# Optimization experiments

Hardware: AMD Instinct MI355X
Metric: run time of the kernel (lower is better)

The kernel has to match this reference:

```python
import jax, jax.numpy as jnp
import numpy as np
import math

E = 256      # embed_dim
H = 16       # num_heads
D = E // H   # qkv_dim
MSH = 16     # ms_hidden_dim
B, R, C = 2, 512, 512


def setup_inputs() -> dict:
    key = jax.random.key(0)
    ks = jax.random.split(key, 10)
    x1 = jax.random.normal(ks[0], (B, R, E), jnp.float32)
    x2 = jax.random.normal(ks[1], (B, C, E), jnp.float32)
    attn_mask = jax.random.randint(ks[2], (B, R, C), 0, 2) > 0  # True = valid
    cost_mat = jax.random.uniform(ks[3], (B, R, C), jnp.float32)
    # torch nn.Linear default init ~ U(-1/sqrt(fan_in), 1/sqrt(fan_in))
    def lin(k, out_d, in_d, bound):
        return jax.random.uniform(k, (out_d, in_d), jnp.float32, -bound, bound)
    Wqv1 = lin(ks[4], 2 * E, E, 1.0 / math.sqrt(E))
    Wkv2 = lin(ks[5], 2 * E, E, 1.0 / math.sqrt(E))
    W1 = lin(ks[6], H * MSH, 2 * H, math.sqrt(0.5))       # mix1_init
    W2 = lin(ks[7], H, H * MSH, math.sqrt(1.0 / MSH))      # mix2_init
    Wout1 = lin(ks[8], E, E, 1.0 / math.sqrt(E))
    Wout2 = lin(ks[9], E, E, 1.0 / math.sqrt(E))
    return {"x1": x1, "x2": x2, "attn_mask": attn_mask, "cost_mat": cost_mat,
            "Wqv1": Wqv1, "Wkv2": Wkv2, "W1": W1, "W2": W2,
            "Wout1": Wout1, "Wout2": Wout2}


def _apply_weights_and_combine(logits, v, mask):
    # mask: True = masked out; rows fully masked are un-masked (torch clone trick)
    all_masked = jnp.all(mask, axis=-1, keepdims=True)
    mask = jnp.where(all_masked, False, mask)
    logits = jnp.where(mask, -jnp.inf, logits)
    w = jax.nn.softmax(logits, axis=-1)          # [b,h,r,c]
    out = jnp.einsum('bhrc,bhcd->bhrd', w, v)     # [b,h,r,d]
    b, h, r, d = out.shape
    return out.transpose(0, 2, 1, 3).reshape(b, r, h * d)  # b s (h d)


def reference(x1, x2, attn_mask, cost_mat, Wqv1, Wkv2, W1, W2, Wout1, Wout2):
    b, r, _ = x1.shape
    c = x2.shape[1]
    # q, v1 from x1 ; k, v2 from x2
    qv = (x1 @ Wqv1.T).reshape(b, r, 2, H, D)
    q = qv[:, :, 0].transpose(0, 2, 1, 3)   # [b,h,r,d]
    v1 = qv[:, :, 1].transpose(0, 2, 1, 3)
    kv = (x2 @ Wkv2.T).reshape(b, c, 2, H, D)
    k = kv[:, :, 0].transpose(0, 2, 1, 3)   # [b,h,c,d]
    v2 = kv[:, :, 1].transpose(0, 2, 1, 3)

    dot = jnp.einsum('bhrd,bhcd->bhrc', q, k) * (1.0 / math.sqrt(D))
    cost = jnp.broadcast_to(cost_mat[:, None], dot.shape)  # [b,h,r,c]

    # MixedScoreFF: stack -> [b,h,r,c,2] -> [b,r,c,2h] -> MLP -> [b,r,c,h]
    two = jnp.stack((dot, cost), axis=-1)
    two = two.transpose(0, 2, 3, 1, 4).reshape(b, r, c, 2 * H)
    ms = jax.nn.relu(two @ W1.T) @ W2.T      # [b,r,c,H]
    ms1 = ms.transpose(0, 3, 1, 2)            # [b,h,r,c]
    ms2 = ms1.transpose(0, 1, 3, 2)           # [b,h,c,r]

    mask1 = jnp.broadcast_to(~attn_mask[:, None], (b, H, r, c))  # True = masked
    mask2 = mask1.transpose(0, 1, 3, 2)

    h1 = _apply_weights_and_combine(ms1, v2, mask1) @ Wout1.T  # [b,r,E]
    h2 = _apply_weights_and_combine(ms2, v1, mask2) @ Wout2.T  # [b,c,E]
    return (h1, h2)
```

## Files before the change

### kernel.cpp

```cpp
#include <hip/hip_runtime.h>
#include <hip/hip_bf16.h>

typedef unsigned int   u32;
typedef unsigned short u16;

typedef __attribute__((ext_vector_type(8))) short    sh8;
typedef __attribute__((ext_vector_type(4))) float    f32x4;
typedef __attribute__((ext_vector_type(8))) _Float16 f16x8;
typedef __attribute__((ext_vector_type(2))) _Float16 f16x2;
typedef __attribute__((ext_vector_type(2))) __fp16   fp16x2raw;

union F16x8 { f16x8 v; uint4 u; f16x2 p[4]; _Float16 h[8]; };
union F16x4u { uint2 u; _Float16 h[4]; };
union F16x2u { u32 u; _Float16 h[2]; };
union CvtU  { fp16x2raw r; f16x2 p; u32 u; };

__device__ __forceinline__ float b2f(u16 u) { union { u32 i; float f; } v; v.i = ((u32)u) << 16; return v.f; }
__device__ __forceinline__ u16   f2b(float f){
  union { float f; u32 i; } v; v.f = f;
  u32 u = v.i;
  u32 r = (u + 0x7fffu + ((u >> 16) & 1u)) >> 16;
  return (u16)r;
}
__device__ __forceinline__ u32 pk2(float a, float b) {
  __hip_bfloat162 h2 = __float22bfloat162_rn(make_float2(a, b));
  union { __hip_bfloat162 h; u32 u; } v; v.h = h2; return v.u;
}
__device__ __forceinline__ f16x2 cvtpk(float a, float b) {
  CvtU c; c.r = __builtin_amdgcn_cvt_pkrtz(a, b); return c.p;
}
__device__ __forceinline__ u32 cvtpku(float a, float b) {
  CvtU c; c.r = __builtin_amdgcn_cvt_pkrtz(a, b); return c.u;
}

__device__ __forceinline__ f32x4 mfma16(uint4 a, uint4 b, f32x4 c) {
  union { uint4 u; sh8 s; } ua, ub;
  ua.u = a; ub.u = b;
  return __builtin_amdgcn_mfma_f32_16x16x32_bf16(ua.s, ub.s, c, 0, 0, 0);
}
__device__ __forceinline__ f32x4 mfma32h(f16x8 a, f16x8 b, f32x4 c) {
  return __builtin_amdgcn_mfma_f32_16x16x32_f16(a, b, c, 0, 0, 0);
}

__device__ __forceinline__ void split8(float4 v0, float4 v1, uint4& hi, uint4& lo) {
  float a[8] = {v0.x, v0.y, v0.z, v0.w, v1.x, v1.y, v1.z, v1.w};
  u32 hw[4], lw[4];
#pragma unroll
  for (int t = 0; t < 4; t++) {
    u32 hp = pk2(a[2 * t], a[2 * t + 1]);
    float r0 = a[2 * t]     - __uint_as_float(hp << 16);
    float r1 = a[2 * t + 1] - __uint_as_float(hp & 0xffff0000u);
    hw[t] = hp;
    lw[t] = pk2(r0, r1);
  }
  hi = make_uint4(hw[0], hw[1], hw[2], hw[3]);
  lo = make_uint4(lw[0], lw[1], lw[2], lw[3]);
}

__global__ void __launch_bounds__(256)
gemm_mf(const float* __restrict__ A0, const float* __restrict__ B0, float* __restrict__ C0,
        const float* __restrict__ A1, const float* __restrict__ B1, float* __restrict__ C1,
        int N, int K) {
  int t = threadIdx.x, L = t & 63, w = t >> 6;
  int cl = L & 15, q = L >> 4;
  int by = blockIdx.y, sel = by >> 4;
  const float* A  = sel ? A1 : A0;
  const float* Bw = sel ? B1 : B0;
  float*       C  = sel ? C1 : C0;
  int m0 = (by & 15) * 64 + w * 16;
  int n0 = blockIdx.x * 16;

  f32x4 acc; acc[0] = 0.f; acc[1] = 0.f; acc[2] = 0.f; acc[3] = 0.f;
  const float* ar = A  + (size_t)(m0 + cl) * K + 8 * q;
  const float* br = Bw + (size_t)(n0 + cl) * K + 8 * q;

  for (int k0 = 0; k0 < K; k0 += 32) {
    float4 av0 = *(const float4*)(ar + k0);
    float4 av1 = *(const float4*)(ar + k0 + 4);
    float4 bv0 = *(const float4*)(br + k0);
    float4 bv1 = *(const float4*)(br + k0 + 4);
    uint4 ahi, alo, bhi, blo;
    split8(av0, av1, ahi, alo);
    split8(bv0, bv1, bhi, blo);
    acc = mfma16(ahi, bhi, acc);
    acc = mfma16(ahi, blo, acc);
    acc = mfma16(alo, bhi, acc);
  }
#pragma unroll
  for (int i = 0; i < 4; i++)
    C[(size_t)(m0 + 4 * q + i) * N + n0 + cl] = acc[i];
}

__global__ void __launch_bounds__(256)
gemm_mf_pack(const float* __restrict__ x1, const float* __restrict__ Wqv1, u16* __restrict__ vh1,
             const float* __restrict__ x2, const float* __restrict__ Wkv2, u16* __restrict__ vh2,
             const float* __restrict__ W1, const float* __restrict__ W2,
             uint4* __restrict__ QQ4, uint4* __restrict__ KH4, uint4* __restrict__ KL4z,
             uint4* __restrict__ W1F8hi, uint4* __restrict__ W1F8lo,
             uint4* __restrict__ W2F8hi, uint4* __restrict__ W2F8lo) {
  __shared__ float Ld[4][16][17];
  int t = threadIdx.x, L = t & 63, w = t >> 6;
  int cl = L & 15, q = L >> 4;
  int by = blockIdx.y;

  if (by == 32) {
    if (blockIdx.x >= 8) return;
    int tid = blockIdx.x * 256 + t;
    if (tid < 1024) {
      int LL = tid & 63, nt = tid >> 6;
      int j = nt * 16 + (LL & 15), qq = LL >> 4;
      F16x8 hi, lo;
#pragma unroll
      for (int jj = 0; jj < 8; jj++) {
        float wv = W1[j * 32 + qq * 8 + jj];
        hi.h[jj] = (_Float16)wv;
        lo.h[jj] = (_Float16)(wv - (float)hi.h[jj]);
      }
      W1F8hi[tid] = hi.u;
      W1F8lo[tid] = lo.u;
    } else if (tid < 1536) {
      int t2 = tid - 1024;
      int LL = t2 & 63, p = t2 >> 6;
      int h = LL & 15, qq = LL >> 4;
      F16x8 hi, lo;
#pragma unroll
      for (int jj = 0; jj < 8; jj++) {
        int j = 32 * p + ((jj >> 2) << 4) + 4 * qq + (jj & 3);
        float wv = W2[h * 256 + j];
        hi.h[jj] = (_Float16)wv;
        lo.h[jj] = (_Float16)(wv - (float)hi.h[jj]);
      }
      W2F8hi[t2] = hi.u;
      W2F8lo[t2] = lo.u;
    }
    return;
  }

  int sel = by >> 4;
  const float* A  = sel ? x2 : x1;
  const float* Bw = sel ? Wkv2 : Wqv1;
  int m0 = (by & 15) * 64 + w * 16;
  int n0 = blockIdx.x * 16;

  f32x4 acc; acc[0] = 0.f; acc[1] = 0.f; acc[2] = 0.f; acc[3] = 0.f;
  const float* ar = A  + (size_t)(m0 + cl) * 256 + 8 * q;
  const float* br = Bw + (size_t)(n0 + cl) * 256 + 8 * q;

  for (int k0 = 0; k0 < 256; k0 += 32) {
    float4 av0 = *(const float4*)(ar + k0);
    float4 av1 = *(const float4*)(ar + k0 + 4);
    float4 bv0 = *(const float4*)(br + k0);
    float4 bv1 = *(const float4*)(br + k0 + 4);
    uint4 ahi, alo, bhi, blo;
    split8(av0, av1, ahi, alo);
    split8(bv0, bv1, bhi, blo);
    acc = mfma16(ahi, bhi, acc);
    acc = mfma16(ahi, blo, acc);
    acc = mfma16(alo, bhi, acc);
  }

  int b = m0 >> 9;
  int row = (m0 & 511) + cl;

  if (n0 >= 256) {
#pragma unroll
    for (int i = 0; i < 4; i++) Ld[w][cl][4 * q + i] = acc[i];
    if (q < 2) {
      float v[8];
#pragma unroll
      for (int jj = 0; jj < 8; jj++) v[jj] = Ld[w][q * 8 + jj][cl];
      uint4 o = make_uint4(cvtpku(v[0], v[1]), cvtpku(v[2], v[3]),
                           cvtpku(v[4], v[5]), cvtpku(v[6], v[7]));
      u16* vh = sel ? vh2 : vh1;
      *(uint4*)(vh + ((size_t)(b * 512) + row) * 256 + (n0 - 256) + q * 8) = o;
    }
    return;
  }

#pragma unroll
  for (int i = 0; i < 4; i++) Ld[w][cl][4 * q + i] = acc[i];
  float v[8];
#pragma unroll
  for (int jj = 0; jj < 8; jj++) v[jj] = Ld[w][(q & 1) * 8 + jj][cl];

  int r = row;
  int h = n0 >> 4;

  if (sel == 0) {
    u32 wv[4];
#pragma unroll
    for (int t2 = 0; t2 < 4; t2++) {
      float a  = v[2 * t2] * 0.25f, bb = v[2 * t2 + 1] * 0.25f;
      u32 hp = pk2(a, bb);
      if (q >= 2) {
        float r0 = a  - __uint_as_float(hp << 16);
        float r1 = bb - __uint_as_float(hp & 0xffff0000u);
        wv[t2] = pk2(r0, r1);
      } else wv[t2] = hp;
    }
    QQ4[((size_t)((b * 16 + h) * 4 + q) << 9) + r] = make_uint4(wv[0], wv[1], wv[2], wv[3]);
  } else {
    u32 hw[4], lw[4];
#pragma unroll
    for (int t2 = 0; t2 < 4; t2++) {
      float a = v[2 * t2], bb = v[2 * t2 + 1];
      u32 hp = pk2(a, bb);
      float r0 = a  - __uint_as_float(hp << 16);
      float r1 = bb - __uint_as_float(hp & 0xffff0000u);
      hw[t2] = hp;
      lw[t2] = pk2(r0, r1);
    }
    if (q < 2) {
      KH4[((size_t)((b * 16 + h) * 2 + q) << 9) + r]       = make_uint4(hw[0], hw[1], hw[2], hw[3]);
      KL4z[((size_t)((b * 16 + h) * 4 + 2 + q) << 9) + r]  = make_uint4(0, 0, 0, 0);
    } else {
      KL4z[((size_t)((b * 16 + h) * 4 + (q - 2)) << 9) + r] = make_uint4(lw[0], lw[1], lw[2], lw[3]);
    }
  }
}

__global__ void __launch_bounds__(256, 4)
ms_mfma8c(const uint4* __restrict__ QQ4, const uint4* __restrict__ KH4,
          const uint4* __restrict__ KL4z, const float* __restrict__ cost,
          const uint4* __restrict__ W1F8hi, const uint4* __restrict__ W1F8lo,
          const uint4* __restrict__ W2F8hi, const uint4* __restrict__ W2F8lo,
          u16* __restrict__ ms1, u16* __restrict__ ms2) {
  __shared__ __align__(16) u32 Dl[2 * 2176];
  int t = threadIdx.x, L = t & 63, w = t >> 6;
  int cl = L & 15, q = L >> 4;
  int b = blockIdx.z, c0 = blockIdx.x * 16;
  int pairId = w >> 1, wl = w & 1;
  int r0a = blockIdx.y * 32 + pairId * 16;
  int r0  = r0a + wl * 8;
  u32* D = Dl + pairId * 2176;

  f32x4 z; z[0] = 0.f; z[1] = 0.f; z[2] = 0.f; z[3] = 0.f;

#pragma unroll 2
  for (int hpi = 0; hpi < 4; hpi++) {
    int hp = wl * 4 + hpi;
    int h0 = 2 * hp, h1 = 2 * hp + 1;
    uint4 qa  = QQ4[((size_t)((b * 16 + h0) * 4 + q) << 9) + r0a + cl];
    uint4 qa2 = QQ4[((size_t)((b * 16 + h0) * 4 + (q & 1)) << 9) + r0a + cl];
    uint4 kb1 = KH4[((size_t)((b * 16 + h0) * 2 + (q & 1)) << 9) + c0 + cl];
    uint4 kb2 = KL4z[((size_t)((b * 16 + h0) * 4 + q) << 9) + c0 + cl];
    f32x4 d0 = mfma16(qa, kb1, z);
    d0 = mfma16(qa2, kb2, d0);
    uint4 qb  = QQ4[((size_t)((b * 16 + h1) * 4 + q) << 9) + r0a + cl];
    uint4 qb2 = QQ4[((size_t)((b * 16 + h1) * 4 + (q & 1)) << 9) + r0a + cl];
    uint4 kc1 = KH4[((size_t)((b * 16 + h1) * 2 + (q & 1)) << 9) + c0 + cl];
    uint4 kc2 = KL4z[((size_t)((b * 16 + h1) * 4 + q) << 9) + c0 + cl];
    f32x4 d1 = mfma16(qb, kc1, z);
    d1 = mfma16(qb2, kc2, d1);
#pragma unroll
    for (int i = 0; i < 4; i++)
      D[(4 * q + i) * 136 + hp * 17 + cl] = cvtpku(d0[i], d1[i]);
  }
  __syncthreads();

  F16x8 xv[8];
#pragma unroll
  for (int rr = 0; rr < 8; rr++) {
    int rl = wl * 8 + rr;
    float cv = cost[((size_t)(b * 512) + r0 + rr) * 512 + c0 + cl];
    u32 ch = cvtpku(0.f, cv);
    u32 ua = D[rl * 136 + (2 * q) * 17 + cl];
    u32 ub = D[rl * 136 + (2 * q + 1) * 17 + cl];
    xv[rr].u = make_uint4((ua & 0xffffu) | ch, (ua >> 16) | ch,
                          (ub & 0xffffu) | ch, (ub >> 16) | ch);
  }

  f32x4 acc2[8];
#pragma unroll
  for (int rr = 0; rr < 8; rr++) acc2[rr] = z;

#pragma unroll 1
  for (int p = 0; p < 8; p++) {
    F16x8 w1h0, w1h1, w2h, w2l;
    w1h0.u = W1F8hi[(2 * p) * 64 + L];
    w1h1.u = W1F8hi[(2 * p + 1) * 64 + L];
    w2h.u  = W2F8hi[p * 64 + L];
    w2l.u  = W2F8lo[p * 64 + L];
#pragma unroll
    for (int rr = 0; rr < 8; rr++) {
      f32x4 a0 = mfma32h(w1h0.v, xv[rr].v, z);
      f32x4 a1 = mfma32h(w1h1.v, xv[rr].v, z);
      F16x8 hf;
      hf.p[0] = cvtpk(fmaxf(a0[0], 0.f), fmaxf(a0[1], 0.f));
      hf.p[1] = cvtpk(fmaxf(a0[2], 0.f), fmaxf(a0[3], 0.f));
      hf.p[2] = cvtpk(fmaxf(a1[0], 0.f), fmaxf(a1[1], 0.f));
      hf.p[3] = cvtpk(fmaxf(a1[2], 0.f), fmaxf(a1[3], 0.f));
      acc2[rr] = mfma32h(hf.v, w2h.v, acc2[rr]);
      acc2[rr] = mfma32h(hf.v, w2l.v, acc2[rr]);
    }
  }

  u32* ms1u = (u32*)ms1;
#pragma unroll
  for (int rr = 0; rr < 8; rr++) {
    size_t base = ((size_t)(b * 16 + cl) * 512 + (r0 + rr)) * 256 + (c0 >> 1) + q * 2;
    ms1u[base]     = pk2(acc2[rr][0], acc2[rr][1]);
    ms1u[base + 1] = pk2(acc2[rr][2], acc2[rr][3]);
  }
  u32* ms2u = (u32*)ms2;
#pragma unroll
  for (int i = 0; i < 4; i++) {
    int c = c0 + 4 * q + i;
    u32 o[4];
#pragma unroll
    for (int j = 0; j < 4; j++)
      o[j] = pk2(acc2[2 * j][i], acc2[2 * j + 1][i]);
    size_t base2 = ((size_t)(b * 16 + cl) * 512 + c) * 256 + (r0 >> 1);
    *(uint4*)&ms2u[base2] = make_uint4(o[0], o[1], o[2], o[3]);
  }
}

__global__ void __launch_bounds__(256)
softmax_all5b(const u16* __restrict__ ms1s, const u16* __restrict__ ms2s,
              const int* __restrict__ mask,
              const u16* __restrict__ vh1, const u16* __restrict__ vh2,
              float* __restrict__ o1, float* __restrict__ o2) {
  __shared__ _Float16 pbuf[512 * 16 * 2];
  __shared__ float    sden[2][16];
  __shared__ float4   red[4][64];
  int t = threadIdx.x, lane = t & 63, w = t >> 6;
  int fix0 = blockIdx.x * 2, b = blockIdx.y, dir = blockIdx.z;
  const u16* ms   = dir ? ms2s : ms1s;
  const u16* vbuf = dir ? vh1 : vh2;
  float*     obuf = dir ? o2 : o1;

  int fsel = w >> 1;
  int fix  = fix0 + fsel;
  int hbase = (w & 1) * 8;
  bool vd[8];
#pragma unroll
  for (int i = 0; i < 8; i++) {
    int cc = i * 64 + lane;
    int mv = dir ? mask[((size_t)b * 512 + cc) * 512 + fix]
                 : mask[((size_t)b * 512 + fix) * 512 + cc];
    vd[i] = mv != 0;
  }
  bool anyl = false;
#pragma unroll
  for (int i = 0; i < 8; i++) anyl |= vd[i];
  bool useMask = (__ballot(anyl) != 0ULL);

#pragma unroll 2
  for (int h2 = 0; h2 < 8; h2++) {
    int h = hbase + h2;
    const u16* mrow = ms + ((size_t)(b * 16 + h) * 512 + fix) * 512;
    float lg[8];
#pragma unroll
    for (int i = 0; i < 8; i++) lg[i] = b2f(mrow[i * 64 + lane]);
    float mx = -3.4e38f;
#pragma unroll
    for (int i = 0; i < 8; i++)
      if (!(useMask && !vd[i])) mx = fmaxf(mx, lg[i]);
    for (int off = 32; off; off >>= 1) mx = fmaxf(mx, __shfl_xor(mx, off));
    float s = 0.f;
#pragma unroll
    for (int i = 0; i < 8; i++) {
      float p = (useMask && !vd[i]) ? 0.f : __expf(lg[i] - mx);
      int cc = i * 64 + lane;
      pbuf[(cc * 16 + ((h + cc) & 15)) * 2 + fsel] = (_Float16)p;
      s += p;
    }
    for (int off = 32; off; off >>= 1) s += __shfl_xor(s, off);
    if (lane == 0) sden[fsel][h] = s;
  }
  __syncthreads();

  int hb = lane >> 2, dq = lane & 3;
  const u16* vb = vbuf + (size_t)b * 131072 + hb * 16 + dq * 4;
  float4 acc0 = make_float4(0.f, 0.f, 0.f, 0.f);
  float4 acc1 = make_float4(0.f, 0.f, 0.f, 0.f);
  for (int it = 0; it < 128; it++) {
    int cc = it * 4 + w;
    F16x4u vv; vv.u = *(const uint2*)(vb + (size_t)cc * 256);
    F16x2u pv; pv.u = *(const u32*)&pbuf[(cc * 16 + ((hb + cc) & 15)) * 2];
    float v0 = (float)vv.h[0], v1 = (float)vv.h[1];
    float v2 = (float)vv.h[2], v3 = (float)vv.h[3];
    float p0 = (float)pv.h[0], p1 = (float)pv.h[1];
    acc0.x += p0 * v0; acc0.y += p0 * v1; acc0.z += p0 * v2; acc0.w += p0 * v3;
    acc1.x += p1 * v0; acc1.y += p1 * v1; acc1.z += p1 * v2; acc1.w += p1 * v3;
  }
#pragma unroll 1
  for (int f = 0; f < 2; f++) {
    red[w][lane] = f ? acc1 : acc0;
    __syncthreads();
    if (w == 0) {
      float4 s0 = red[0][lane], s1 = red[1][lane];
      float4 s2 = red[2][lane], s3 = red[3][lane];
      float inv = 1.f / sden[f][hb];
      float4 o;
      o.x = (s0.x + s1.x + s2.x + s3.x) * inv;
      o.y = (s0.y + s1.y + s2.y + s3.y) * inv;
      o.z = (s0.z + s1.z + s2.z + s3.z) * inv;
      o.w = (s0.w + s1.w + s2.w + s3.w) * inv;
      *(float4*)(obuf + ((size_t)b * 512 + fix0 + f) * 256 + lane * 4) = o;
    }
    __syncthreads();
  }
}

extern "C" void kernel_launch(void* const* d_in, const int* in_sizes, int n_in,
                              void* d_out, int out_size, void* d_ws, size_t ws_size,
                              hipStream_t stream) {
  const float* x1    = (const float*)d_in[0];
  const float* x2    = (const float*)d_in[1];
  const int*   attn  = (const int*)d_in[2];
  const float* cost  = (const float*)d_in[3];
  const float* Wqv1  = (const float*)d_in[4];
  const float* Wkv2  = (const float*)d_in[5];
  const float* W1    = (const float*)d_in[6];
  const float* W2    = (const float*)d_in[7];
  const float* Wout1 = (const float*)d_in[8];
  const float* Wout2 = (const float*)d_in[9];
  float* out = (float*)d_out;

  char* ws = (char*)d_ws;
  uint4* W1F8hi = (uint4*)(ws);
  uint4* W1F8lo = (uint4*)(ws + (16 << 10));
  uint4* W2F8hi = (uint4*)(ws + (32 << 10));
  uint4* W2F8lo = (uint4*)(ws + (40 << 10));
  u16*   vh1 = (u16*)(ws + (64 << 10));
  u16*   vh2 = (u16*)(ws + (64 << 10) + (512 << 10));
  u16*   ms1 = (u16*)(ws + (64 << 10) + (4 << 20));
  u16*   ms2 = (u16*)(ws + (64 << 10) + (20 << 20));
  char*  tail= (ws + (64 << 10) + (36 << 20));
  uint4* QQ4  = (uint4*)(tail);
  uint4* KH4  = (uint4*)(tail + (1 << 20));
  uint4* KL4z = (uint4*)(tail + (1 << 20) + (512 << 10));
  float* o1  = (float*)(tail + (3 << 20));
  float* o2  = (float*)(tail + (4 << 20));

  gemm_mf_pack<<<dim3(32, 33), 256, 0, stream>>>(x1, Wqv1, vh1, x2, Wkv2, vh2,
                                                 W1, W2, QQ4, KH4, KL4z,
                                                 W1F8hi, W1F8lo, W2F8hi, W2F8lo);

  ms_mfma8c<<<dim3(32, 16, 2), 256, 0, stream>>>(QQ4, KH4, KL4z, cost,
                                                 W1F8hi, W1F8lo, W2F8hi, W2F8lo, ms1, ms2);

  softmax_all5b<<<dim3(256, 2, 2), 256, 0, stream>>>(ms1, ms2, attn, vh1, vh2, o1, o2);

  gemm_mf<<<dim3(16, 32), 256, 0, stream>>>(o1, Wout1, out, o2, Wout2, out + (size_t)262144, 256, 256);
}
```

Measured before the change: 157.7 us.

## Compute softmax P·V with MFMA using transposed V and bit-packed mask

The softmax kernel is restructured so each block handles 8 rows and 4 heads (one head per wave). Probabilities are written to an XOR-swizzled LDS tile and multiplied against V with f16 MFMA instructions instead of scalar FMA loops. To make this possible, the QKV projection kernel now stores V transposed (head-dim major, sequence contiguous). The mask is packed into bytes in LDS with vectorized loads. This removes the scalar PV inner loop and the cross-wave reduction, at the cost of a new transposed layout and more complex indexing.

```diff
diff --git a/kernel.cpp b/kernel.cpp
--- a/kernel.cpp
+++ b/kernel.cpp
@@ -92,8 +92,8 @@
 }
 
 __global__ void __launch_bounds__(256)
-gemm_mf_pack(const float* __restrict__ x1, const float* __restrict__ Wqv1, u16* __restrict__ vh1,
-             const float* __restrict__ x2, const float* __restrict__ Wkv2, u16* __restrict__ vh2,
+gemm_mf_pack(const float* __restrict__ x1, const float* __restrict__ Wqv1, u16* __restrict__ vhT1,
+             const float* __restrict__ x2, const float* __restrict__ Wkv2, u16* __restrict__ vhT2,
              const float* __restrict__ W1, const float* __restrict__ W2,
              uint4* __restrict__ QQ4, uint4* __restrict__ KH4, uint4* __restrict__ KL4z,
              uint4* __restrict__ W1F8hi, uint4* __restrict__ W1F8lo,
@@ -166,13 +166,13 @@
 #pragma unroll
     for (int i = 0; i < 4; i++) Ld[w][cl][4 * q + i] = acc[i];
     if (q < 2) {
-      float v[8];
-#pragma unroll
-      for (int jj = 0; jj < 8; jj++) v[jj] = Ld[w][q * 8 + jj][cl];
-      uint4 o = make_uint4(cvtpku(v[0], v[1]), cvtpku(v[2], v[3]),
-                           cvtpku(v[4], v[5]), cvtpku(v[6], v[7]));
-      u16* vh = sel ? vh2 : vh1;
-      *(uint4*)(vh + ((size_t)(b * 512) + row) * 256 + (n0 - 256) + q * 8) = o;
+      float vt[8];
+#pragma unroll
+      for (int jj = 0; jj < 8; jj++) vt[jj] = Ld[w][cl][q * 8 + jj];
+      uint4 o = make_uint4(cvtpku(vt[0], vt[1]), cvtpku(vt[2], vt[3]),
+                           cvtpku(vt[4], vt[5]), cvtpku(vt[6], vt[7]));
+      u16* vT = sel ? vhT2 : vhT1;
+      *(uint4*)(vT + ((size_t)(b * 256) + (n0 - 256) + cl) * 512 + (m0 & 511) + 8 * q) = o;
     }
     return;
   }
@@ -315,91 +315,105 @@
   }
 }
 
-__global__ void __launch_bounds__(256)
-softmax_all5b(const u16* __restrict__ ms1s, const u16* __restrict__ ms2s,
+__global__ void __launch_bounds__(256, 4)
+softmax_pv_mf(const u16* __restrict__ ms1s, const u16* __restrict__ ms2s,
               const int* __restrict__ mask,
-              const u16* __restrict__ vh1, const u16* __restrict__ vh2,
+              const u16* __restrict__ vhT1, const u16* __restrict__ vhT2,
               float* __restrict__ o1, float* __restrict__ o2) {
-  __shared__ _Float16 pbuf[512 * 16 * 2];
-  __shared__ float    sden[2][16];
-  __shared__ float4   red[4][64];
-  int t = threadIdx.x, lane = t & 63, w = t >> 6;
-  int fix0 = blockIdx.x * 2, b = blockIdx.y, dir = blockIdx.z;
-  const u16* ms   = dir ? ms2s : ms1s;
-  const u16* vbuf = dir ? vh1 : vh2;
-  float*     obuf = dir ? o2 : o1;
-
-  int fsel = w >> 1;
-  int fix  = fix0 + fsel;
-  int hbase = (w & 1) * 8;
-  bool vd[8];
-#pragma unroll
-  for (int i = 0; i < 8; i++) {
-    int cc = i * 64 + lane;
-    int mv = dir ? mask[((size_t)b * 512 + cc) * 512 + fix]
-                 : mask[((size_t)b * 512 + fix) * 512 + cc];
-    vd[i] = mv != 0;
-  }
-  bool anyl = false;
-#pragma unroll
-  for (int i = 0; i < 8; i++) anyl |= vd[i];
-  bool useMask = (__ballot(anyl) != 0ULL);
-
-#pragma unroll 2
-  for (int h2 = 0; h2 < 8; h2++) {
-    int h = hbase + h2;
-    const u16* mrow = ms + ((size_t)(b * 16 + h) * 512 + fix) * 512;
+  __shared__ __align__(16) char pbufc[4][8192];
+  __shared__ unsigned char maskbytes[8][64];
+  __shared__ float sden[4][8];
+  int t = threadIdx.x, L = t & 63, w = t >> 6;
+  int cl = L & 15, q = L >> 4;
+  int rt = blockIdx.x >> 2, hq = blockIdx.x & 3;
+  int b = blockIdx.y, dir = blockIdx.z;
+  int fix0 = rt * 8, h = hq * 4 + w;
+  const u16* ms = dir ? ms2s : ms1s;
+
+  if (dir == 0) {
+#pragma unroll
+    for (int fo = 0; fo < 2; fo++) {
+      int f = 2 * w + fo;
+      const int* mr = mask + ((size_t)(b * 512) + fix0 + f) * 512 + 8 * L;
+      uint4 m0 = *(const uint4*)mr;
+      uint4 m1 = *(const uint4*)(mr + 4);
+      u32 bits = (u32)(m0.x != 0)        | ((u32)(m0.y != 0) << 1)
+               | ((u32)(m0.z != 0) << 2) | ((u32)(m0.w != 0) << 3)
+               | ((u32)(m1.x != 0) << 4) | ((u32)(m1.y != 0) << 5)
+               | ((u32)(m1.z != 0) << 6) | ((u32)(m1.w != 0) << 7);
+      maskbytes[f][L] = (unsigned char)bits;
+    }
+  } else {
+    u32 b0 = 0, b1 = 0;
+#pragma unroll
+    for (int j = 0; j < 8; j++) {
+      const int* mp = mask + ((size_t)(b * 512) + 8 * L + j) * 512 + fix0 + 2 * w;
+      uint2 mv = *(const uint2*)mp;
+      b0 |= (u32)(mv.x != 0) << j;
+      b1 |= (u32)(mv.y != 0) << j;
+    }
+    maskbytes[2 * w][L]     = (unsigned char)b0;
+    maskbytes[2 * w + 1][L] = (unsigned char)b1;
+  }
+  __syncthreads();
+
+  const u16* msbase = ms + ((size_t)((b * 16 + h) * 512) + fix0) * 512 + 8 * L;
+  uint4 pre[8];
+#pragma unroll
+  for (int f = 0; f < 8; f++) pre[f] = *(const uint4*)(msbase + f * 512);
+
+  char* pb = pbufc[w];
+#pragma unroll
+  for (int f = 0; f < 8; f++) {
+    u32 uw[4] = {pre[f].x, pre[f].y, pre[f].z, pre[f].w};
     float lg[8];
 #pragma unroll
-    for (int i = 0; i < 8; i++) lg[i] = b2f(mrow[i * 64 + lane]);
+    for (int j = 0; j < 4; j++) {
+      lg[2 * j]     = __uint_as_float(uw[j] << 16);
+      lg[2 * j + 1] = __uint_as_float(uw[j] & 0xffff0000u);
+    }
+    u32 mb = (u32)maskbytes[f][L];
+    bool um = (__ballot(mb != 0) != 0ULL);
+    u32 eff = um ? mb : 0xffu;
     float mx = -3.4e38f;
 #pragma unroll
-    for (int i = 0; i < 8; i++)
-      if (!(useMask && !vd[i])) mx = fmaxf(mx, lg[i]);
+    for (int j = 0; j < 8; j++)
+      mx = fmaxf(mx, ((eff >> j) & 1) ? lg[j] : -3.4e38f);
     for (int off = 32; off; off >>= 1) mx = fmaxf(mx, __shfl_xor(mx, off));
-    float s = 0.f;
-#pragma unroll
-    for (int i = 0; i < 8; i++) {
-      float p = (useMask && !vd[i]) ? 0.f : __expf(lg[i] - mx);
-      int cc = i * 64 + lane;
-      pbuf[(cc * 16 + ((h + cc) & 15)) * 2 + fsel] = (_Float16)p;
-      s += p;
+    float s = 0.f; u32 pw[4];
+#pragma unroll
+    for (int j = 0; j < 4; j++) {
+      float p0 = ((eff >> (2 * j)) & 1)     ? __expf(lg[2 * j]     - mx) : 0.f;
+      float p1 = ((eff >> (2 * j + 1)) & 1) ? __expf(lg[2 * j + 1] - mx) : 0.f;
+      s += p0 + p1;
+      pw[j] = cvtpku(p0, p1);
     }
     for (int off = 32; off; off >>= 1) s += __shfl_xor(s, off);
-    if (lane == 0) sden[fsel][h] = s;
-  }
-  __syncthreads();
-
-  int hb = lane >> 2, dq = lane & 3;
-  const u16* vb = vbuf + (size_t)b * 131072 + hb * 16 + dq * 4;
-  float4 acc0 = make_float4(0.f, 0.f, 0.f, 0.f);
-  float4 acc1 = make_float4(0.f, 0.f, 0.f, 0.f);
-  for (int it = 0; it < 128; it++) {
-    int cc = it * 4 + w;
-    F16x4u vv; vv.u = *(const uint2*)(vb + (size_t)cc * 256);
-    F16x2u pv; pv.u = *(const u32*)&pbuf[(cc * 16 + ((hb + cc) & 15)) * 2];
-    float v0 = (float)vv.h[0], v1 = (float)vv.h[1];
-    float v2 = (float)vv.h[2], v3 = (float)vv.h[3];
-    float p0 = (float)pv.h[0], p1 = (float)pv.h[1];
-    acc0.x += p0 * v0; acc0.y += p0 * v1; acc0.z += p0 * v2; acc0.w += p0 * v3;
-    acc1.x += p1 * v0; acc1.y += p1 * v1; acc1.z += p1 * v2; acc1.w += p1 * v3;
-  }
-#pragma unroll 1
-  for (int f = 0; f < 2; f++) {
-    red[w][lane] = f ? acc1 : acc0;
-    __syncthreads();
-    if (w == 0) {
-      float4 s0 = red[0][lane], s1 = red[1][lane];
-      float4 s2 = red[2][lane], s3 = red[3][lane];
-      float inv = 1.f / sden[f][hb];
-      float4 o;
-      o.x = (s0.x + s1.x + s2.x + s3.x) * inv;
-      o.y = (s0.y + s1.y + s2.y + s3.y) * inv;
-      o.z = (s0.z + s1.z + s2.z + s3.z) * inv;
-      o.w = (s0.w + s1.w + s2.w + s3.w) * inv;
-      *(float4*)(obuf + ((size_t)b * 512 + fix0 + f) * 256 + lane * 4) = o;
-    }
-    __syncthreads();
+    if (L == 0) sden[w][f] = s;
+    *(uint4*)(pb + f * 1024 + ((16 * L) ^ (f << 4))) = make_uint4(pw[0], pw[1], pw[2], pw[3]);
+  }
+
+  const u16* vT = (dir ? vhT1 : vhT2) + ((size_t)(b * 256 + h * 16 + cl) * 512) + 8 * q;
+  f32x4 accA; accA[0] = 0.f; accA[1] = 0.f; accA[2] = 0.f; accA[3] = 0.f;
+  f32x4 accB = accA;
+  int ar = (cl & 7);
+#pragma unroll
+  for (int kk = 0; kk < 16; kk++) {
+    F16x8 pa, vb;
+    pa.u = *(const uint4*)(pb + ar * 1024 + (((kk << 6) + (q << 4)) ^ (ar << 4)));
+    vb.u = *(const uint4*)(vT + (kk << 5));
+    if (kk & 1) accB = mfma32h(pa.v, vb.v, accB);
+    else        accA = mfma32h(pa.v, vb.v, accA);
+  }
+
+  if (q < 2) {
+    float* obuf = dir ? o2 : o1;
+#pragma unroll
+    for (int i = 0; i < 4; i++) {
+      int f = 4 * q + i;
+      float inv = 1.f / sden[w][f];
+      obuf[((size_t)(b * 512) + fix0 + f) * 256 + h * 16 + cl] = (accA[i] + accB[i]) * inv;
+    }
   }
 }
 
@@ -423,8 +437,8 @@
   uint4* W1F8lo = (uint4*)(ws + (16 << 10));
   uint4* W2F8hi = (uint4*)(ws + (32 << 10));
   uint4* W2F8lo = (uint4*)(ws + (40 << 10));
-  u16*   vh1 = (u16*)(ws + (64 << 10));
-  u16*   vh2 = (u16*)(ws + (64 << 10) + (512 << 10));
+  u16*   vhT1 = (u16*)(ws + (64 << 10));
+  u16*   vhT2 = (u16*)(ws + (64 << 10) + (512 << 10));
   u16*   ms1 = (u16*)(ws + (64 << 10) + (4 << 20));
   u16*   ms2 = (u16*)(ws + (64 << 10) + (20 << 20));
   char*  tail= (ws + (64 << 10) + (36 << 20));
@@ -434,14 +448,14 @@
   float* o1  = (float*)(tail + (3 << 20));
   float* o2  = (float*)(tail + (4 << 20));
 
-  gemm_mf_pack<<<dim3(32, 33), 256, 0, stream>>>(x1, Wqv1, vh1, x2, Wkv2, vh2,
+  gemm_mf_pack<<<dim3(32, 33), 256, 0, stream>>>(x1, Wqv1, vhT1, x2, Wkv2, vhT2,
                                                  W1, W2, QQ4, KH4, KL4z,
                                                  W1F8hi, W1F8lo, W2F8hi, W2F8lo);
 
   ms_mfma8c<<<dim3(32, 16, 2), 256, 0, stream>>>(QQ4, KH4, KL4z, cost,
                                                  W1F8hi, W1F8lo, W2F8hi, W2F8lo, ms1, ms2);
 
-  softmax_all5b<<<dim3(256, 2, 2), 256, 0, stream>>>(ms1, ms2, attn, vh1, vh2, o1, o2);
+  softmax_pv_mf<<<dim3(256, 2, 2), 256, 0, stream>>>(ms1, ms2, attn, vhT1, vhT2, o1, o2);
 
   gemm_mf<<<dim3(16, 32), 256, 0, stream>>>(o1, Wout1, out, o2, Wout2, out + (size_t)262144, 256, 256);
 }
```

Result: faster. 145.8 us (-7.5%).
